# Performance work log

Measured on AMD Instinct MI355X. Metric: run time of the kernel, lower is better.

Reference implementation:

```python
import jax, jax.numpy as jnp
import numpy as np

NEG_SLOPE = 0.2


def gat_conv(feat, src, dst, W, al, ar, num_nodes, activation):
    # feat: [N, F_in]; W: [F_in, H*D]; al, ar: [H, D]
    H, D = al.shape
    h = (feat @ W).reshape(-1, H, D)                      # [N, H, D]
    el = jnp.sum(h * al, axis=-1)                         # [N, H]
    er = jnp.sum(h * ar, axis=-1)                         # [N, H]
    e = jax.nn.leaky_relu(el[src] + er[dst], NEG_SLOPE)   # [E, H]
    # edge softmax over incoming edges of each destination node
    emax = jax.ops.segment_max(e, dst, num_segments=num_nodes)   # [N, H]
    ee = jnp.exp(e - emax[dst])                           # [E, H]
    denom = jax.ops.segment_sum(ee, dst, num_segments=num_nodes)  # [N, H]
    alpha = ee / jnp.maximum(denom[dst], 1e-9)            # [E, H]
    msg = h[src] * alpha[:, :, None]                      # [E, H, D]
    out = jax.ops.segment_sum(msg, dst, num_segments=num_nodes)   # [N, H, D]
    return activation(out) if activation is not None else out


def setup_inputs() -> dict:
    key = jax.random.key(0)
    ks = jax.random.split(key, 12)
    N, E, F_IN, HID, C = 100000, 1600000, 256, 32, 40
    heads = [4, 4, 1]
    inp = {
        "feats": jax.random.normal(ks[0], (N, F_IN), dtype=jnp.float32),
        "src": jax.random.randint(ks[1], (E,), 0, N, dtype=jnp.int32),
        "dst": jax.random.randint(ks[2], (E,), 0, N, dtype=jnp.int32),
    }
    def glorot(k, shape):
        fan = shape[0] + shape[-1]
        return jax.random.normal(k, shape, dtype=jnp.float32) * np.sqrt(2.0 / fan)
    # layer 0: in=256 -> heads[0]*HID
    inp["W0"] = glorot(ks[3], (F_IN, heads[0] * HID))
    inp["al0"] = glorot(ks[4], (heads[0], HID))
    inp["ar0"] = glorot(ks[5], (heads[0], HID))
    # layer 1: in=heads[0]*HID -> heads[1]*HID
    inp["W1"] = glorot(ks[6], (heads[0] * HID, heads[1] * HID))
    inp["al1"] = glorot(ks[7], (heads[1], HID))
    inp["ar1"] = glorot(ks[8], (heads[1], HID))
    # output layer: in=heads[1]*HID -> heads[2]*C
    inp["W2"] = glorot(ks[9], (heads[1] * HID, heads[2] * C))
    inp["al2"] = glorot(ks[10], (heads[2], C))
    inp["ar2"] = glorot(ks[11], (heads[2], C))
    return inp


def reference(feats, src, dst, W0, al0, ar0, W1, al1, ar1, W2, al2, ar2):
    N = feats.shape[0]
    elu = jax.nn.elu
    h1 = gat_conv(feats, src, dst, W0, al0, ar0, N, elu).reshape(N, -1)  # flatten(1)
    h2 = gat_conv(h1, src, dst, W1, al1, ar1, N, elu).reshape(N, -1)
    logits = gat_conv(h2, src, dst, W2, al2, ar2, N, None).mean(axis=1)  # mean over heads
    return (logits, h1, h2)
```

## Files before the change

### kernel.cpp

```cpp
#include <hip/hip_runtime.h>
#include <hip/hip_bf16.h>
#include <hip/hip_fp16.h>

#define NEG_SLOPE 0.2f
#define BW 256
#define MAXB 512

typedef __attribute__((ext_vector_type(8))) short short8;
typedef __attribute__((ext_vector_type(4))) float f32x4;

__device__ inline float bf2f(short s) {
    union { unsigned u; float f; } v;
    v.u = ((unsigned)(unsigned short)s) << 16;
    return v.f;
}
__device__ inline short f2bf(float f) {
    __hip_bfloat16 h = __float2bfloat16(f);
    return (short)*reinterpret_cast<unsigned short*>(&h);
}
__device__ inline float lo_bf(unsigned u) {
    union { unsigned u; float f; } v;
    v.u = u << 16;
    return v.f;
}
__device__ inline float hi_bf(unsigned u) {
    union { unsigned u; float f; } v;
    v.u = u & 0xFFFF0000u;
    return v.f;
}
__device__ inline unsigned pack_sb(int s, float p) {
    union { float f; unsigned u; } v;
    v.f = p;
    return ((unsigned)s << 15) | ((v.u >> 16) & 0x7FFFu);
}
__device__ inline float unpack_b(unsigned u) {
    union { unsigned u; float f; } v;
    v.u = (u & 0x7FFFu) << 16;
    return v.f;
}
__device__ inline void gload16(const void* g, void* lds) {
    __builtin_amdgcn_global_load_lds((const __attribute__((address_space(1))) void*)g,
                                     (__attribute__((address_space(3))) void*)lds, 16, 0, 0);
}


__global__ __launch_bounds__(256) void bhist_kernel(const int* __restrict__ dst,
                                                    int* __restrict__ bcnt, int E, int NB) {
    __shared__ int h[MAXB];
    int tid = threadIdx.x;
    for (int i = tid; i < NB; i += 256) h[i] = 0;
    __syncthreads();
    int e0 = blockIdx.x * 4096;
#pragma unroll
    for (int i = 0; i < 16; ++i) {
        int e = e0 + i * 256 + tid;
        if (e < E) atomicAdd(&h[dst[e] >> 8], 1);
    }
    __syncthreads();
    for (int i = tid; i < NB; i += 256)
        if (h[i]) atomicAdd(&bcnt[i], h[i]);
}

__global__ __launch_bounds__(512) void bscan_kernel(const int* __restrict__ bcnt,
                                                    int* __restrict__ bbase,
                                                    int* __restrict__ bcur, int NB, int E) {
    __shared__ int lds[512];
    int tid = threadIdx.x;
    int v = (tid < NB) ? bcnt[tid] : 0;
    lds[tid] = v;
    __syncthreads();
    int x = v;
    for (int off = 1; off < 512; off <<= 1) {
        int y = (tid >= off) ? lds[tid - off] : 0;
        __syncthreads();
        x += y;
        lds[tid] = x;
        __syncthreads();
    }
    int excl = x - v;
    if (tid < NB) {
        bbase[tid] = excl;
        bcur[tid] = excl;
    }
    if (tid == 0) bbase[NB] = E;
}

__global__ __launch_bounds__(256) void bpart_kernel(const int* __restrict__ dst,
                                                    const int* __restrict__ src,
                                                    int* __restrict__ bcur,
                                                    unsigned* __restrict__ tmp, int E, int NB) {
    __shared__ int h[MAXB], h2[MAXB], base[MAXB];
    int tid = threadIdx.x;
    for (int i = tid; i < NB; i += 256) { h[i] = 0; h2[i] = 0; }
    __syncthreads();
    int e0 = blockIdx.x * 4096;
    unsigned pk[16];
    short bb[16];
#pragma unroll
    for (int i = 0; i < 16; ++i) {
        int e = e0 + i * 256 + tid;
        bool valid = e < E;
        int d = valid ? dst[e] : 0;
        int s = valid ? src[e] : 0;
        bb[i] = valid ? (short)(d >> 8) : (short)-1;
        pk[i] = (unsigned)s | ((unsigned)(d & 255) << 17);
        if (valid) atomicAdd(&h[d >> 8], 1);
    }
    __syncthreads();
    for (int i = tid; i < NB; i += 256)
        base[i] = h[i] ? atomicAdd(&bcur[i], h[i]) : 0;
    __syncthreads();
#pragma unroll
    for (int i = 0; i < 16; ++i) {
        if (bb[i] >= 0) {
            int p = base[bb[i]] + atomicAdd(&h2[bb[i]], 1);
            tmp[p] = pk[i];
        }
    }
}

__global__ __launch_bounds__(256) void bsort_kernel(const unsigned* __restrict__ tmp,
                                                    const int* __restrict__ bbase,
                                                    int* __restrict__ csr,
                                                    int* __restrict__ offsets, int N, int NB) {
    __shared__ int cnt[BW], cur[BW];
    int b = blockIdx.x;
    int tid = threadIdx.x;
    int Rb = bbase[b], Rend = bbase[b + 1];
    cnt[tid] = 0;
    __syncthreads();
    for (int i = Rb + tid; i < Rend; i += 256) atomicAdd(&cnt[tmp[i] >> 17], 1);
    __syncthreads();
    int v = cnt[tid];
    cur[tid] = v;
    __syncthreads();
    int x = v;
    for (int off = 1; off < 256; off <<= 1) {
        int y = (tid >= off) ? cur[tid - off] : 0;
        __syncthreads();
        x += y;
        cur[tid] = x;
        __syncthreads();
    }
    int excl = x - v;
    int g = b * BW + tid;
    if (g <= N) offsets[g] = Rb + excl;
    cur[tid] = Rb + excl;
    __syncthreads();
    for (int i = Rb + tid; i < Rend; i += 256) {
        unsigned p = tmp[i];
        int pos = atomicAdd(&cur[p >> 17], 1);
        csr[pos] = (int)(p & 0x1FFFFu);
    }
}


__global__ __launch_bounds__(256) void cvtT2_kernel(const float* __restrict__ W0,
                                                    __hip_bfloat16* __restrict__ Wt0,
                                                    const float* __restrict__ W1,
                                                    __hip_bfloat16* __restrict__ Wt1) {
    int i = blockIdx.x * 256 + threadIdx.x;
    if (i < 256 * 128) {
        int k = i / 128, n = i % 128;
        Wt0[(size_t)n * 256 + k] = __float2bfloat16(W0[i]);
    } else if (i < 256 * 128 + 128 * 128) {
        int j = i - 256 * 128;
        int k = j / 128, n = j % 128;
        Wt1[(size_t)n * 128 + k] = __float2bfloat16(W1[j]);
    }
}


template <bool CVT_A>
__global__ __launch_bounds__(256) void gemm_mfma(const void* __restrict__ Av,
                                                 const __hip_bfloat16* __restrict__ Bt,
                                                 __hip_bfloat16* __restrict__ Cb,
                                                 int M, int K) {
    __shared__ __align__(16) short smem[8192];
    const int tid = threadIdx.x;
    const int lane = tid & 63;
    const int w = tid >> 6;
    const int wr = w >> 1, wc = w & 1;
    const int bm = blockIdx.x * 128;
    f32x4 acc[4][4];
#pragma unroll
    for (int m = 0; m < 4; ++m)
#pragma unroll
        for (int n = 0; n < 4; ++n) acc[m][n] = 0.f;

    for (int k0 = 0; k0 < K; k0 += 32) {
#pragma unroll
        for (int i = 0; i < 2; ++i) {
            const int c = (w * 2 + i) * 64 + lane;
            const int row = c >> 2;
            const int kpg = (c & 3) ^ (row & 3);
            int grow = bm + row;
            grow = grow < M ? grow : M - 1;
            if (CVT_A) {
                const float* gp = (const float*)Av + (size_t)grow * K + k0 + kpg * 8;
                f32x4 f0 = __builtin_nontemporal_load((const f32x4*)gp);
                f32x4 f1 = __builtin_nontemporal_load((const f32x4*)(gp + 4));
                short8 v;
                v[0] = f2bf(f0[0]); v[1] = f2bf(f0[1]); v[2] = f2bf(f0[2]); v[3] = f2bf(f0[3]);
                v[4] = f2bf(f1[0]); v[5] = f2bf(f1[1]); v[6] = f2bf(f1[2]); v[7] = f2bf(f1[3]);
                *(short8*)&smem[c * 8] = v;
            } else {
                const __hip_bfloat16* gp =
                    (const __hip_bfloat16*)Av + (size_t)grow * K + k0 + kpg * 8;
                gload16(gp, &smem[(w * 2 + i) * 512]);
            }
        }
#pragma unroll
        for (int i = 0; i < 2; ++i) {
            const int c = (w * 2 + i) * 64 + lane;
            const int col = c >> 2;
            const int kpg = (c & 3) ^ (col & 3);
            const __hip_bfloat16* gp = Bt + (size_t)col * K + k0 + kpg * 8;
            gload16(gp, &smem[4096 + (w * 2 + i) * 512]);
        }
        __syncthreads();
        short8 a[4], b[4];
        const int kp = lane >> 4;
#pragma unroll
        for (int m = 0; m < 4; ++m) {
            const int row = wr * 64 + m * 16 + (lane & 15);
            a[m] = *(const short8*)&smem[row * 32 + ((kp ^ (row & 3)) << 3)];
        }
#pragma unroll
        for (int n = 0; n < 4; ++n) {
            const int col = wc * 64 + n * 16 + (lane & 15);
            b[n] = *(const short8*)&smem[4096 + col * 32 + ((kp ^ (col & 3)) << 3)];
        }
#pragma unroll
        for (int m = 0; m < 4; ++m)
#pragma unroll
            for (int n = 0; n < 4; ++n)
                acc[m][n] = __builtin_amdgcn_mfma_f32_16x16x32_bf16(a[m], b[n], acc[m][n], 0, 0, 0);
        __syncthreads();
    }
#pragma unroll
    for (int m = 0; m < 4; ++m)
#pragma unroll
        for (int j = 0; j < 4; ++j) {
            int row = bm + wr * 64 + m * 16 + (lane >> 4) * 4 + j;
            if (row >= M) continue;
#pragma unroll
            for (int n = 0; n < 4; ++n) {
                int col = wc * 64 + n * 16 + (lane & 15);
                Cb[(size_t)row * 128 + col] = __float2bfloat16(acc[m][n][j]);
            }
        }
}


__global__ __launch_bounds__(256) void gemm40_kernel(const __hip_bfloat16* __restrict__ A,
                                                     const float* __restrict__ W,
                                                     const float* __restrict__ al,
                                                     const float* __restrict__ ar,
                                                     __hip_bfloat16* __restrict__ C,
                                                     float* __restrict__ el,
                                                     float* __restrict__ er, int M) {
    int rowb = blockIdx.x * 256 + threadIdx.x;
    int row = rowb < M ? rowb : M - 1;
    float acc[40];
#pragma unroll
    for (int c = 0; c < 40; ++c) acc[c] = 0.f;
    const short8* ap = (const short8*)(A + (size_t)row * 128);
#pragma unroll 1
    for (int kc = 0; kc < 16; ++kc) {
        short8 v = ap[kc];
#pragma unroll
        for (int j = 0; j < 8; ++j) {
            float f = bf2f(v[j]);
            const float* wrow = W + (kc * 8 + j) * 40;
#pragma unroll
            for (int c = 0; c < 40; ++c) acc[c] += f * wrow[c];
        }
    }
    if (rowb < M) {
        float sl = 0.f, sr = 0.f;
#pragma unroll
        for (int c = 0; c < 40; ++c) {
            __hip_bfloat16 hb = __float2bfloat16(acc[c]);
            float hv = __bfloat162float(hb);
            C[(size_t)rowb * 64 + c] = hb;
            sl += hv * al[c];
            sr += hv * ar[c];
        }
#pragma unroll
        for (int c = 40; c < 64; ++c) C[(size_t)rowb * 64 + c] = __float2bfloat16(0.f);
        el[rowb] = sl;
        er[rowb] = sr;
    }
}


__global__ __launch_bounds__(256) void eler4_kernel(const __hip_bfloat16* __restrict__ h,
                                                    const float* __restrict__ al,
                                                    const float* __restrict__ ar,
                                                    float* __restrict__ el,
                                                    float* __restrict__ er, int NH) {
    int idx = blockIdx.x * 256 + threadIdx.x;
    if (idx >= NH) return;
    int hh = idx & 3;
    const short8* hp = (const short8*)(h + (size_t)idx * 32);
    float sl = 0.f, sr = 0.f;
#pragma unroll
    for (int ck = 0; ck < 4; ++ck) {
        short8 v = hp[ck];
#pragma unroll
        for (int j = 0; j < 8; ++j) {
            float f = bf2f(v[j]);
            sl += f * al[hh * 32 + ck * 8 + j];
            sr += f * ar[hh * 32 + ck * 8 + j];
        }
    }
    el[idx] = sl;
    er[idx] = sr;
}


__global__ __launch_bounds__(256) void gat_agg4_kernel(
    const int* __restrict__ offsets, const int* __restrict__ csr_src,
    const float* __restrict__ el, const float* __restrict__ er,
    const __hip_bfloat16* __restrict__ hfeat, float* __restrict__ outf,
    unsigned* __restrict__ outb, int N) {
    int node = blockIdx.x * 4 + (threadIdx.x >> 6);
    if (node >= N) return;
    int lane = threadIdx.x & 63;
    int ha = lane & 3;
    int es = lane >> 2;
    int cl = lane & 31;
    int half = lane >> 5;
    int h2 = cl >> 3;
    int beg = offsets[node], end = offsets[node + 1];
    float ern = er[node * 4 + ha];
    float d_acc = 0.f;
    float acc[4] = {0.f, 0.f, 0.f, 0.f};
    const __hip_bfloat16* hcol = hfeat + cl * 4;
    for (int base = beg; base < end; base += 16) {
        int b = base + es;
        bool valid = b < end;
        int s = valid ? csr_src[b] : 0;
        float x = -1e30f;
        if (valid) {
            x = el[s * 4 + ha] + ern;
            x = x > 0.f ? x : NEG_SLOPE * x;
        }
        float p = __expf(x);
        float pv[8];
        int rv[8];
#pragma unroll
        for (int k = 0; k < 8; ++k) {
            int e = half + 2 * k;
            pv[k] = __shfl(p, (e << 2) | h2);
            rv[k] = __shfl(s, e << 2);
        }
        ushort4 hv[8];
#pragma unroll
        for (int k = 0; k < 8; ++k)
            hv[k] = *(const ushort4*)(hcol + (size_t)rv[k] * 128);
#pragma unroll
        for (int k = 0; k < 8; ++k) {
            float a = pv[k];
            d_acc += a;
            unsigned w0 = (unsigned)hv[k].x | ((unsigned)hv[k].y << 16);
            unsigned w1 = (unsigned)hv[k].z | ((unsigned)hv[k].w << 16);
            acc[0] += lo_bf(w0) * a;
            acc[1] += hi_bf(w0) * a;
            acc[2] += lo_bf(w1) * a;
            acc[3] += hi_bf(w1) * a;
        }
    }
#pragma unroll
    for (int j = 0; j < 4; ++j) acc[j] += __shfl_xor(acc[j], 32);
    d_acc += __shfl_xor(d_acc, 32);
    float idn = 1.f / fmaxf(d_acc, 1e-9f);
    if (half == 0) {
        float v[4];
#pragma unroll
        for (int j = 0; j < 4; ++j) {
            float t = acc[j] * idn;
            v[j] = t > 0.f ? t : __expf(t) - 1.f;
        }
        f32x4 fo = {v[0], v[1], v[2], v[3]};
        *(f32x4*)(outf + (size_t)node * 128 + cl * 4) = fo;
        unsigned u0 = (unsigned short)f2bf(v[0]) | ((unsigned)(unsigned short)f2bf(v[1]) << 16);
        unsigned u1 = (unsigned short)f2bf(v[2]) | ((unsigned)(unsigned short)f2bf(v[3]) << 16);
        uint2 uo = {u0, u1};
        *(uint2*)(outb + (size_t)node * 64 + cl * 2) = uo;
    }
}


__global__ __launch_bounds__(256) void gat_agg1_kernel(
    const int* __restrict__ offsets, const int* __restrict__ csr_src,
    const float* __restrict__ el, const float* __restrict__ er,
    const __hip_bfloat16* __restrict__ hfeat, float* __restrict__ logits, int N) {
    int node = blockIdx.x * 4 + (threadIdx.x >> 6);
    if (node >= N) return;
    int lane = threadIdx.x & 63;
    int cl = lane & 31;
    int half = lane >> 5;
    bool active = cl < 20;
    int beg = offsets[node], end = offsets[node + 1];
    float ern = er[node];
    float d_acc = 0.f;
    float acc0 = 0.f, acc1 = 0.f;
    const __hip_bfloat16* hcol = hfeat + cl * 2;
    for (int base = beg; base < end; base += 64) {
        int b = base + lane;
        bool valid = b < end;
        int s = valid ? csr_src[b] : 0;
        float x = -1e30f;
        if (valid) {
            x = el[s] + ern;
            x = x > 0.f ? x : NEG_SLOPE * x;
        }
        float p = __expf(x);
        unsigned u_mine = pack_sb(s, p);
        int cnt = min(64, end - base);
        for (int sb = 0; sb < cnt; sb += 16) {
            unsigned uk[8];
#pragma unroll
            for (int k = 0; k < 8; ++k) {
                int e = sb + half + 2 * k;
                uk[k] = __shfl(u_mine, e & 63);
                if (e >= cnt) uk[k] &= ~0x7FFFu;
            }
            unsigned hv[8];
#pragma unroll
            for (int k = 0; k < 8; ++k)
                hv[k] = active ? *(const unsigned*)(hcol + ((size_t)(uk[k] >> 15)) * 64) : 0u;
#pragma unroll
            for (int k = 0; k < 8; ++k) {
                float a = unpack_b(uk[k]);
                d_acc += a;
                acc0 += lo_bf(hv[k]) * a;
                acc1 += hi_bf(hv[k]) * a;
            }
        }
    }
    acc0 += __shfl_xor(acc0, 32);
    acc1 += __shfl_xor(acc1, 32);
    d_acc += __shfl_xor(d_acc, 32);
    float idn = 1.f / fmaxf(d_acc, 1e-9f);
    if (half == 0 && active) {
        float2 fo = {acc0 * idn, acc1 * idn};
        *(float2*)(logits + (size_t)node * 40 + cl * 2) = fo;
    }
}


extern "C" void kernel_launch(void* const* d_in, const int* in_sizes, int n_in,
                              void* d_out, int out_size, void* d_ws, size_t ws_size,
                              hipStream_t stream) {
    const float* feats = (const float*)d_in[0];
    const int* src = (const int*)d_in[1];
    const int* dst = (const int*)d_in[2];
    const float* W0 = (const float*)d_in[3];
    const float* al0 = (const float*)d_in[4];
    const float* ar0 = (const float*)d_in[5];
    const float* W1 = (const float*)d_in[6];
    const float* al1 = (const float*)d_in[7];
    const float* ar1 = (const float*)d_in[8];
    const float* W2 = (const float*)d_in[9];
    const float* al2 = (const float*)d_in[10];
    const float* ar2 = (const float*)d_in[11];

    const int N = in_sizes[0] / 256;
    const int E = in_sizes[1];
    const int NB = (N + BW - 1) / BW;

    float* out = (float*)d_out;
    float* logits = out;
    float* h1 = out + (size_t)N * 40;
    float* h2 = h1 + (size_t)N * 128;

    char* p = (char*)d_ws;
    __hip_bfloat16* hA = (__hip_bfloat16*)p; p += (size_t)N * 128 * 2;
    __hip_bfloat16* hB = (__hip_bfloat16*)p; p += (size_t)N * 128 * 2;
    float* el = (float*)p;   p += (size_t)N * 4 * 4;
    float* er = (float*)p;   p += (size_t)N * 4 * 4;
    __hip_bfloat16* Wt0 = (__hip_bfloat16*)p; p += 128 * 256 * 2;
    __hip_bfloat16* Wt1 = (__hip_bfloat16*)p; p += 128 * 128 * 2;
    int* offsets = (int*)p;  p += (size_t)(N + 1) * 4;
    int* bcnt = (int*)p;     p += MAXB * 4;
    int* bbase = (int*)p;    p += (MAXB + 1) * 4;
    int* bcur = (int*)p;     p += MAXB * 4;
    int* csr = (int*)p;      p += (size_t)E * 4;
    unsigned* tmp = (unsigned*)hA;

    const int gN256 = (N + 255) / 256;
    const int gE4096 = (E + 4095) / 4096;
    const int gM128 = (N + 127) / 128;
    const int gAgg = (N + 3) / 4;

    hipMemsetAsync(bcnt, 0, MAXB * sizeof(int), stream);
    bhist_kernel<<<gE4096, 256, 0, stream>>>(dst, bcnt, E, NB);
    bscan_kernel<<<1, 512, 0, stream>>>(bcnt, bbase, bcur, NB, E);
    bpart_kernel<<<gE4096, 256, 0, stream>>>(dst, src, bcur, tmp, E, NB);
    bsort_kernel<<<NB, 256, 0, stream>>>(tmp, bbase, csr, offsets, N, NB);

    cvtT2_kernel<<<(256 * 128 + 128 * 128 + 255) / 256, 256, 0, stream>>>(W0, Wt0, W1, Wt1);

    gemm_mfma<true><<<gM128, 256, 0, stream>>>(feats, Wt0, hA, N, 256);
    eler4_kernel<<<(N * 4 + 255) / 256, 256, 0, stream>>>(hA, al0, ar0, el, er, N * 4);
    gat_agg4_kernel<<<gAgg, 256, 0, stream>>>(offsets, csr, el, er, hA, h1, (unsigned*)hB, N);

    gemm_mfma<false><<<gM128, 256, 0, stream>>>(hB, Wt1, hA, N, 128);
    eler4_kernel<<<(N * 4 + 255) / 256, 256, 0, stream>>>(hA, al1, ar1, el, er, N * 4);
    gat_agg4_kernel<<<gAgg, 256, 0, stream>>>(offsets, csr, el, er, hA, h2, (unsigned*)hB, N);

    gemm40_kernel<<<gN256, 256, 0, stream>>>(hB, W2, al2, ar2, hA, el, er, N);
    gat_agg1_kernel<<<gAgg, 256, 0, stream>>>(offsets, csr, el, er, hA, logits, N);
}
```

Measured before the change: 389.3 us.

## Fuse attention-logit computation into MFMA GEMM epilogue and use nontemporal output stores

Computes el/er per row and head inside the GEMM epilogue from the fp32 accumulators, using 16-lane shuffle reductions, so the separate eler4 kernels and their re-read of h are gone. The aggregation kernels' final fp32 outputs now use nontemporal stores to avoid polluting cache. A side effect is that el/er are now computed from fp32 accumulators rather than bf16-rounded h, which changes numerics slightly. It also adds shuffle work to the GEMM epilogue.

```diff
diff --git a/kernel.cpp b/kernel.cpp
--- a/kernel.cpp
+++ b/kernel.cpp
@@ -8,6 +8,7 @@
 
 typedef __attribute__((ext_vector_type(8))) short short8;
 typedef __attribute__((ext_vector_type(4))) float f32x4;
+typedef __attribute__((ext_vector_type(2))) float f32x2;
 
 __device__ inline float bf2f(short s) {
     union { unsigned u; float f; } v;
@@ -175,6 +176,10 @@
 __global__ __launch_bounds__(256) void gemm_mfma(const void* __restrict__ Av,
                                                  const __hip_bfloat16* __restrict__ Bt,
                                                  __hip_bfloat16* __restrict__ Cb,
+                                                 const float* __restrict__ al,
+                                                 const float* __restrict__ ar,
+                                                 float* __restrict__ el,
+                                                 float* __restrict__ er,
                                                  int M, int K) {
     __shared__ __align__(16) short smem[8192];
     const int tid = threadIdx.x;
@@ -250,6 +255,35 @@
                 Cb[(size_t)row * 128 + col] = __float2bfloat16(acc[m][n][j]);
             }
         }
+    const int lx = lane & 15;
+    const float al00 = al[2 * wc * 32 + lx],        al01 = al[2 * wc * 32 + 16 + lx];
+    const float al10 = al[(2 * wc + 1) * 32 + lx],  al11 = al[(2 * wc + 1) * 32 + 16 + lx];
+    const float ar00 = ar[2 * wc * 32 + lx],        ar01 = ar[2 * wc * 32 + 16 + lx];
+    const float ar10 = ar[(2 * wc + 1) * 32 + lx],  ar11 = ar[(2 * wc + 1) * 32 + 16 + lx];
+#pragma unroll
+    for (int m = 0; m < 4; ++m) {
+#pragma unroll
+        for (int j = 0; j < 4; ++j) {
+            int row = bm + wr * 64 + m * 16 + (lane >> 4) * 4 + j;
+            float pl0 = acc[m][0][j] * al00 + acc[m][1][j] * al01;
+            float pr0 = acc[m][0][j] * ar00 + acc[m][1][j] * ar01;
+            float pl1 = acc[m][2][j] * al10 + acc[m][3][j] * al11;
+            float pr1 = acc[m][2][j] * ar10 + acc[m][3][j] * ar11;
+#pragma unroll
+            for (int off = 1; off < 16; off <<= 1) {
+                pl0 += __shfl_xor(pl0, off);
+                pr0 += __shfl_xor(pr0, off);
+                pl1 += __shfl_xor(pl1, off);
+                pr1 += __shfl_xor(pr1, off);
+            }
+            if (lx == 0 && row < M) {
+                el[row * 4 + 2 * wc] = pl0;
+                el[row * 4 + 2 * wc + 1] = pl1;
+                er[row * 4 + 2 * wc] = pr0;
+                er[row * 4 + 2 * wc + 1] = pr1;
+            }
+        }
+    }
 }
 
 
@@ -292,31 +326,6 @@
         el[rowb] = sl;
         er[rowb] = sr;
     }
-}
-
-
-__global__ __launch_bounds__(256) void eler4_kernel(const __hip_bfloat16* __restrict__ h,
-                                                    const float* __restrict__ al,
-                                                    const float* __restrict__ ar,
-                                                    float* __restrict__ el,
-                                                    float* __restrict__ er, int NH) {
-    int idx = blockIdx.x * 256 + threadIdx.x;
-    if (idx >= NH) return;
-    int hh = idx & 3;
-    const short8* hp = (const short8*)(h + (size_t)idx * 32);
-    float sl = 0.f, sr = 0.f;
-#pragma unroll
-    for (int ck = 0; ck < 4; ++ck) {
-        short8 v = hp[ck];
-#pragma unroll
-        for (int j = 0; j < 8; ++j) {
-            float f = bf2f(v[j]);
-            sl += f * al[hh * 32 + ck * 8 + j];
-            sr += f * ar[hh * 32 + ck * 8 + j];
-        }
-    }
-    el[idx] = sl;
-    er[idx] = sr;
 }
 
 
@@ -384,7 +393,7 @@
             v[j] = t > 0.f ? t : __expf(t) - 1.f;
         }
         f32x4 fo = {v[0], v[1], v[2], v[3]};
-        *(f32x4*)(outf + (size_t)node * 128 + cl * 4) = fo;
+        __builtin_nontemporal_store(fo, (f32x4*)(outf + (size_t)node * 128 + cl * 4));
         unsigned u0 = (unsigned short)f2bf(v[0]) | ((unsigned)(unsigned short)f2bf(v[1]) << 16);
         unsigned u1 = (unsigned short)f2bf(v[2]) | ((unsigned)(unsigned short)f2bf(v[3]) << 16);
         uint2 uo = {u0, u1};
@@ -446,8 +455,8 @@
     d_acc += __shfl_xor(d_acc, 32);
     float idn = 1.f / fmaxf(d_acc, 1e-9f);
     if (half == 0 && active) {
-        float2 fo = {acc0 * idn, acc1 * idn};
-        *(float2*)(logits + (size_t)node * 40 + cl * 2) = fo;
+        f32x2 fo = {acc0 * idn, acc1 * idn};
+        __builtin_nontemporal_store(fo, (f32x2*)(logits + (size_t)node * 40 + cl * 2));
     }
 }
 
@@ -496,7 +505,8 @@
     const int gM128 = (N + 127) / 128;
     const int gAgg = (N + 3) / 4;
 
-    hipMemsetAsync(bcnt, 0, MAXB * sizeof(int), stream);
+    hipError_t _e = hipMemsetAsync(bcnt, 0, MAXB * sizeof(int), stream);
+    (void)_e;
     bhist_kernel<<<gE4096, 256, 0, stream>>>(dst, bcnt, E, NB);
     bscan_kernel<<<1, 512, 0, stream>>>(bcnt, bbase, bcur, NB, E);
     bpart_kernel<<<gE4096, 256, 0, stream>>>(dst, src, bcur, tmp, E, NB);
@@ -504,12 +514,10 @@
 
     cvtT2_kernel<<<(256 * 128 + 128 * 128 + 255) / 256, 256, 0, stream>>>(W0, Wt0, W1, Wt1);
 
-    gemm_mfma<true><<<gM128, 256, 0, stream>>>(feats, Wt0, hA, N, 256);
-    eler4_kernel<<<(N * 4 + 255) / 256, 256, 0, stream>>>(hA, al0, ar0, el, er, N * 4);
+    gemm_mfma<true><<<gM128, 256, 0, stream>>>(feats, Wt0, hA, al0, ar0, el, er, N, 256);
     gat_agg4_kernel<<<gAgg, 256, 0, stream>>>(offsets, csr, el, er, hA, h1, (unsigned*)hB, N);
 
-    gemm_mfma<false><<<gM128, 256, 0, stream>>>(hB, Wt1, hA, N, 128);
-    eler4_kernel<<<(N * 4 + 255) / 256, 256, 0, stream>>>(hA, al1, ar1, el, er, N * 4);
+    gemm_mfma<false><<<gM128, 256, 0, stream>>>(hB, Wt1, hA, al1, ar1, el, er, N, 128);
     gat_agg4_kernel<<<gAgg, 256, 0, stream>>>(offsets, csr, el, er, hA, h2, (unsigned*)hB, N);
 
     gemm40_kernel<<<gN256, 256, 0, stream>>>(hB, W2, al2, ar2, hA, el, er, N);
```

New measurement: 374.1 us. 1.04x faster.
